# Kernel optimization log

Hardware: AMD Instinct MI355X
Metric: run time of the kernel (lower is better)

## Reference

```python
import jax, jax.numpy as jnp
import numpy as np

MOMENTUM = 0.999
TEMP = 0.07
NUM_HARD_NEGS = 16
NUM_CLASSES = 20000


def _normalize(x, axis=-1, eps=1e-12):
    n = jnp.linalg.norm(x, axis=axis, keepdims=True)
    return x / jnp.maximum(n, eps)


def setup_inputs() -> dict:
    key = jax.random.key(0)
    k1, k2, k3, k4, k5 = jax.random.split(key, 5)
    B, K, Dp, De, C = 512, 8, 256, 512, NUM_CLASSES
    return {
        "part_features": jax.random.normal(k1, (B, K, Dp), dtype=jnp.float32),
        "embeddings": jax.random.normal(k2, (B, De), dtype=jnp.float32),
        "sat_emb": jax.random.normal(k3, (B, De), dtype=jnp.float32),
        "part_bank": jax.random.normal(k4, (C, K, Dp), dtype=jnp.float32) * 0.01,
        "embed_bank": jax.random.normal(k5, (C, De), dtype=jnp.float32) * 0.01,
        "labels": jnp.arange(B, dtype=jnp.int64),
    }


def reference(part_features, embeddings, sat_emb, part_bank, embed_bank, labels):
    m = MOMENTUM
    B = embeddings.shape[0]
    C = embed_bank.shape[0]

    # --- EMA scatter update (bank assumed initialized for all classes) ---
    # labels are distinct, so vectorized scatter == sequential python loop.
    new_part_bank = part_bank.at[labels].set(
        m * part_bank[labels] + (1.0 - m) * part_features)
    new_embed_bank = embed_bank.at[labels].set(
        m * embed_bank[labels] + (1.0 - m) * embeddings)

    # Banks are torch buffers updated under no_grad -> stop_gradient.
    eb = jax.lax.stop_gradient(new_embed_bank)

    # --- PrototypeNCE ---
    q = _normalize(embeddings)                      # [B, De]
    protos = _normalize(eb)                         # [C, De]
    sim = (q @ protos.T) / TEMP                     # [B, C]
    pos_sim = jnp.take_along_axis(sim, labels[:, None], axis=1)  # [B, 1]
    class_ids = jnp.arange(C)
    pos_mask = labels[:, None] == class_ids[None, :]
    neg_sim = jnp.where(pos_mask, -1e9, sim)
    hard_negs, _ = jax.lax.top_k(neg_sim, NUM_HARD_NEGS)          # [B, k]
    logits = jnp.concatenate([pos_sim, hard_negs], axis=1)       # [B, 1+k]
    nce_loss = jnp.mean(jax.nn.logsumexp(logits, axis=1) - logits[:, 0])

    # --- Cross-view prototype alignment ---
    p = _normalize(eb[labels])                      # [B, De]
    d = _normalize(embeddings)
    s = _normalize(sat_emb)
    align_loss = 0.5 * (jnp.mean(1.0 - jnp.sum(d * p, axis=-1))
                        + jnp.mean(1.0 - jnp.sum(s * p, axis=-1)))

    return new_part_bank, new_embed_bank, nce_loss, align_loss
```

## Files before the change

kernel.cpp:

```cpp
#include <hip/hip_runtime.h>
#include <math.h>

#define MOM 0.999f
#define ONE_M_MOM 0.001f
#define INV_TEMP (1.0f / 0.07f)
#define C_CLASSES 20000
#define B_SZ 512
#define DE 512
#define PART_ROW 2048
#define PART_BANK_N (C_CLASSES * PART_ROW)
#define EMB_BANK_N (C_CLASSES * DE)
#define NEG_INF (-3.0e38f)
#define NTILE 157
#define NGEMM (4 * NTILE)
#define NCHUNK 2500

typedef __attribute__((ext_vector_type(8))) short short8;
typedef __attribute__((ext_vector_type(4))) float f32x4;

__device__ inline unsigned short f2bf_rne(float f) {
    unsigned u = __builtin_bit_cast(unsigned, f);
    return (unsigned short)((u + 0x7FFFu + ((u >> 16) & 1u)) >> 16);
}

__device__ inline float bf2f(unsigned short u) {
    return __builtin_bit_cast(float, (unsigned)u << 16);
}

__device__ inline void gload16(const void* g, void* l) {
    __builtin_amdgcn_global_load_lds(
        (const __attribute__((address_space(1))) unsigned int*)g,
        (__attribute__((address_space(3))) unsigned int*)l, 16, 0, 0);
}

__global__ void __launch_bounds__(256)
embed_qnorm(const float* __restrict__ ebank, const float* __restrict__ emb,
            const int* __restrict__ labels, float* __restrict__ out_eb,
            float* __restrict__ inv_norm, unsigned short* __restrict__ Ab,
            int* __restrict__ counter) {
    int blk = blockIdx.x;
    int t = threadIdx.x;
    if (blk == 0 && t == 0) *counter = 0;
    int w = t >> 6, l = t & 63;
    if (blk < 5000) {
        int c = blk * 4 + w;
        int m = -1;
#pragma unroll
        for (int k = 0; k < 8; ++k)
            if (labels[l + k * 64] == c) m = l + k * 64;
#pragma unroll
        for (int off = 32; off; off >>= 1) m = max(m, __shfl_xor(m, off));

        const float4* row = (const float4*)(ebank + ((long)c << 9));
        float4 v0 = row[2 * l], v1 = row[2 * l + 1];
        if (m >= 0) {
            const float4* nr = (const float4*)(emb + ((long)m << 9));
            float4 n0 = nr[2 * l], n1 = nr[2 * l + 1];
            v0.x = MOM * v0.x + ONE_M_MOM * n0.x;
            v0.y = MOM * v0.y + ONE_M_MOM * n0.y;
            v0.z = MOM * v0.z + ONE_M_MOM * n0.z;
            v0.w = MOM * v0.w + ONE_M_MOM * n0.w;
            v1.x = MOM * v1.x + ONE_M_MOM * n1.x;
            v1.y = MOM * v1.y + ONE_M_MOM * n1.y;
            v1.z = MOM * v1.z + ONE_M_MOM * n1.z;
            v1.w = MOM * v1.w + ONE_M_MOM * n1.w;
        }
        float4* orow = (float4*)(out_eb + ((long)c << 9));
        orow[2 * l] = v0; orow[2 * l + 1] = v1;
        float ss = v0.x * v0.x + v0.y * v0.y + v0.z * v0.z + v0.w * v0.w
                 + v1.x * v1.x + v1.y * v1.y + v1.z * v1.z + v1.w * v1.w;
#pragma unroll
        for (int off = 32; off; off >>= 1) ss += __shfl_xor(ss, off);
        if (l == 0) inv_norm[c] = 1.0f / fmaxf(sqrtf(ss), 1e-12f);
    } else {
        int b = (blk - 5000) * 4 + w;
        const float4* row = (const float4*)(emb + ((long)b << 9));
        float4 v0 = row[2 * l], v1 = row[2 * l + 1];
        float ss = v0.x * v0.x + v0.y * v0.y + v0.z * v0.z + v0.w * v0.w
                 + v1.x * v1.x + v1.y * v1.y + v1.z * v1.z + v1.w * v1.w;
#pragma unroll
        for (int off = 32; off; off >>= 1) ss += __shfl_xor(ss, off);
        float inv = 1.0f / fmaxf(sqrtf(ss), 1e-12f);
        v0.x *= inv; v0.y *= inv; v0.z *= inv; v0.w *= inv;
        v1.x *= inv; v1.y *= inv; v1.z *= inv; v1.w *= inv;
        short8 o;
        o[0] = (short)f2bf_rne(v0.x); o[1] = (short)f2bf_rne(v0.y);
        o[2] = (short)f2bf_rne(v0.z); o[3] = (short)f2bf_rne(v0.w);
        o[4] = (short)f2bf_rne(v1.x); o[5] = (short)f2bf_rne(v1.y);
        o[6] = (short)f2bf_rne(v1.z); o[7] = (short)f2bf_rne(v1.w);
        *(short8*)(Ab + ((long)b << 9) + l * 8) = o;
    }
}

__global__ void __launch_bounds__(256)
part_gemm(const unsigned short* __restrict__ A, const float* __restrict__ out_eb,
          const float* __restrict__ inv_norm, const int* __restrict__ labels,
          float* __restrict__ partials,
          const float* __restrict__ pb, const float* __restrict__ pf,
          float* __restrict__ out_pb) {
    __shared__ unsigned short smem[128 * 130];

    if (blockIdx.x >= NGEMM) {
        int c0 = (blockIdx.x - NGEMM) * 8;
        int t = threadIdx.x;
        int* mbs = (int*)smem;
        if (t < 8) mbs[t] = -1;
        __syncthreads();
        int la = labels[t], lb = labels[t + 256];
#pragma unroll
        for (int r = 0; r < 8; ++r) {
            if (la == c0 + r) mbs[r] = t;
            if (lb == c0 + r) mbs[r] = t + 256;
        }
        __syncthreads();
        const f32x4* src = (const f32x4*)pb + (long)c0 * (PART_ROW / 4);
        f32x4* dst = (f32x4*)out_pb + (long)c0 * (PART_ROW / 4);
        const f32x4* pf4 = (const f32x4*)pf;
        f32x4 v[16];
#pragma unroll
        for (int i = 0; i < 16; ++i)
            v[i] = __builtin_nontemporal_load(&src[t + i * 256]);
#pragma unroll
        for (int i = 0; i < 16; ++i) {
            int mb = mbs[i >> 1];
            if (mb >= 0) {
                f32x4 n = pf4[(long)mb * (PART_ROW / 4) + (t + (i & 1) * 256)];
                v[i] = MOM * v[i] + ONE_M_MOM * n;
            }
            __builtin_nontemporal_store(v[i], &dst[t + i * 256]);
        }
        return;
    }

    unsigned short* Asm = smem;
    unsigned short* Bsm = smem + 8192;

    const int t = threadIdx.x;
    const int w = t >> 6, l = t & 63;
    const int wr = w >> 1, wc = w & 1;

    int id = blockIdx.x;
    int xcd = id & 7, idx = id >> 3;
    int wg = (xcd < 4) ? xcd * 79 + idx : 316 + (xcd - 4) * 78 + idx;
    const int bm = wg & 3, bn = wg >> 2;

    f32x4 acc[4][4] = {};

    const int srow = t >> 3;
    const long swz = ((t & 7) ^ (srow & 7)) << 3;
    const unsigned short* Ag = A + ((long)(bm * 128 + srow) << 9) + swz;
    char* Adst = (char*)Asm + (w << 10);

    const int brow = t >> 1;
    const int bh = t & 1;
    int gbr = bn * 128 + brow; if (gbr > C_CLASSES - 1) gbr = C_CLASSES - 1;
    const float4* Bsrc = (const float4*)out_eb + ((long)gbr << 7);
    unsigned short* Bwp = Bsm + (brow << 6);

    const int fr = l & 15;
    const int s4 = l >> 4;
    const int swr0 = ((s4) ^ (fr & 7)) << 4;
    const int swr1 = ((4 + s4) ^ (fr & 7)) << 4;

    for (int kt = 0; kt < 8; ++kt) {
        const int ko = kt << 6;
#pragma unroll
        for (int i = 0; i < 4; ++i)
            gload16(Ag + ko + ((long)i << 14), Adst + (i << 12));
        float4 bv[8];
#pragma unroll
        for (int i = 0; i < 8; ++i) bv[i] = Bsrc[kt * 16 + bh * 8 + i];
#pragma unroll
        for (int s = 0; s < 4; ++s) {
            short8 o;
            float4 x0 = bv[2 * s], x1 = bv[2 * s + 1];
            o[0] = (short)f2bf_rne(x0.x); o[1] = (short)f2bf_rne(x0.y);
            o[2] = (short)f2bf_rne(x0.z); o[3] = (short)f2bf_rne(x0.w);
            o[4] = (short)f2bf_rne(x1.x); o[5] = (short)f2bf_rne(x1.y);
            o[6] = (short)f2bf_rne(x1.z); o[7] = (short)f2bf_rne(x1.w);
            int slot = (bh * 4 + s) ^ (brow & 7);
            *(short8*)(Bwp + slot * 8) = o;
        }
        __syncthreads();
        short8 af[2][4], bf[2][4];
        const char* Abase = (const char*)Asm;
        const char* Bbase = (const char*)Bsm;
#pragma unroll
        for (int m = 0; m < 4; ++m) {
            int ra = (wr * 64 + m * 16 + fr) << 7;
            int rb = (wc * 64 + m * 16 + fr) << 7;
            af[0][m] = *(const short8*)(Abase + ra + swr0);
            af[1][m] = *(const short8*)(Abase + ra + swr1);
            bf[0][m] = *(const short8*)(Bbase + rb + swr0);
            bf[1][m] = *(const short8*)(Bbase + rb + swr1);
        }
        __builtin_amdgcn_s_setprio(1);
#pragma unroll
        for (int kk = 0; kk < 2; ++kk)
#pragma unroll
            for (int m = 0; m < 4; ++m)
#pragma unroll
                for (int n = 0; n < 4; ++n)
                    acc[m][n] = __builtin_amdgcn_mfma_f32_16x16x32_bf16(
                        af[kk][m], bf[kk][n], acc[m][n], 0, 0, 0);
        __builtin_amdgcn_s_setprio(0);
        __syncthreads();
    }

    unsigned short* stile = smem;
    const int r4 = s4 << 2;
#pragma unroll
    for (int n = 0; n < 4; ++n) {
        int ct = wc * 64 + fr + n * 16;
        int cg = bn * 128 + ct;
        bool ok = cg < C_CLASSES;
        float sc = ok ? inv_norm[cg] * INV_TEMP : 0.0f;
#pragma unroll
        for (int m = 0; m < 4; ++m) {
            int rt = wr * 64 + r4 + m * 16;
#pragma unroll
            for (int j = 0; j < 4; ++j) {
                float v = ok ? acc[m][n][j] * sc : NEG_INF;
                stile[(rt + j) * 130 + ct] = f2bf_rne(v);
            }
        }
    }
    __syncthreads();

    const int r = t >> 1, half = t & 1;
    const int gr = bm * 128 + r;
    const int lab = labels[gr];
    const int lab_l = lab - (bn << 7) - (half << 6);
    const unsigned short* bp = stile + r * 130 + half * 64;
    float tl[16];
#pragma unroll
    for (int j = 0; j < 16; ++j) tl[j] = NEG_INF;
    for (int c = 0; c < 64; ++c) {
        if (c == lab_l) continue;
        float v = bf2f(bp[c]);
        if (v > tl[15]) {
            tl[15] = v;
#pragma unroll
            for (int j = 15; j > 0; --j) {
                float a = tl[j - 1], bb = tl[j];
                if (bb > a) { tl[j - 1] = bb; tl[j] = a; }
            }
        }
    }
    float ol[16];
#pragma unroll
    for (int j = 0; j < 16; ++j) ol[j] = __shfl_xor(tl[j], 1);
    if (half == 0) {
        float4 o0, o1, o2, o3;
        o0.x = fmaxf(tl[0],  ol[15]); o0.y = fmaxf(tl[1],  ol[14]);
        o0.z = fmaxf(tl[2],  ol[13]); o0.w = fmaxf(tl[3],  ol[12]);
        o1.x = fmaxf(tl[4],  ol[11]); o1.y = fmaxf(tl[5],  ol[10]);
        o1.z = fmaxf(tl[6],  ol[9]);  o1.w = fmaxf(tl[7],  ol[8]);
        o2.x = fmaxf(tl[8],  ol[7]);  o2.y = fmaxf(tl[9],  ol[6]);
        o2.z = fmaxf(tl[10], ol[5]);  o2.w = fmaxf(tl[11], ol[4]);
        o3.x = fmaxf(tl[12], ol[3]);  o3.y = fmaxf(tl[13], ol[2]);
        o3.z = fmaxf(tl[14], ol[1]);  o3.w = fmaxf(tl[15], ol[0]);
        float4* op4 = (float4*)(partials + ((long)gr * NTILE + bn) * 16);
        op4[0] = o0; op4[1] = o1; op4[2] = o2; op4[3] = o3;
    }
}

__global__ void __launch_bounds__(64)
merge_fin(const float* __restrict__ partials, const float* __restrict__ emb,
          const float* __restrict__ out_eb, const float* __restrict__ sat,
          const float* __restrict__ inv_norm, const int* __restrict__ labels,
          float* __restrict__ lnce, float* __restrict__ lalign,
          int* __restrict__ counter, float* __restrict__ out_losses) {
    int b = blockIdx.x;
    int l = threadIdx.x;
    const float4* pr4 = (const float4*)(partials + (long)b * (NTILE * 16));

    float tl[16];
#pragma unroll
    for (int j = 0; j < 16; ++j) tl[j] = NEG_INF;
    for (int i = l; i < NTILE * 4; i += 64) {
        float4 v4 = pr4[i];
        float vv[4] = {v4.x, v4.y, v4.z, v4.w};
#pragma unroll
        for (int q = 0; q < 4; ++q) {
            float v = vv[q];
            if (v > tl[15]) {
                tl[15] = v;
#pragma unroll
                for (int j = 15; j > 0; --j) {
                    float a = tl[j - 1], bb = tl[j];
                    if (bb > a) { tl[j - 1] = bb; tl[j] = a; }
                }
            }
        }
    }

    float M = 0.f, S = 0.f;
#pragma unroll 1
    for (int j = 0; j < 16; ++j) {
        float v = tl[0];
        float mx = v;
#pragma unroll
        for (int off = 32; off; off >>= 1) mx = fmaxf(mx, __shfl_xor(mx, off));
        unsigned long long ball = __ballot(v == mx);
        int win = (int)(__ffsll((unsigned long long)ball)) - 1;
        if (l == win) {
#pragma unroll
            for (int q = 0; q < 15; ++q) tl[q] = tl[q + 1];
            tl[15] = NEG_INF;
        }
        if (j == 0) { M = mx; S = 1.0f; }
        else S += expf(mx - M);
    }

    int lab = labels[b];
    const float4* qr = (const float4*)(emb + ((long)b << 9));
    const float4* er = (const float4*)(out_eb + ((long)lab << 9));
    const float4* sr = (const float4*)(sat + ((long)b << 9));
    float a1 = 0.f, a2 = 0.f, a3 = 0.f, a4 = 0.f;
#pragma unroll
    for (int rr = 0; rr < 2; ++rr) {
        int j = 2 * l + rr;
        float4 d4 = qr[j], s4 = sr[j], e4 = er[j];
        a1 += d4.x * e4.x + d4.y * e4.y + d4.z * e4.z + d4.w * e4.w;
        a2 += s4.x * e4.x + s4.y * e4.y + s4.z * e4.z + s4.w * e4.w;
        a3 += s4.x * s4.x + s4.y * s4.y + s4.z * s4.z + s4.w * s4.w;
        a4 += d4.x * d4.x + d4.y * d4.y + d4.z * d4.z + d4.w * d4.w;
    }
#pragma unroll
    for (int off = 32; off; off >>= 1) {
        a1 += __shfl_xor(a1, off);
        a2 += __shfl_xor(a2, off);
        a3 += __shfl_xor(a3, off);
        a4 += __shfl_xor(a4, off);
    }
    int done = 0;
    if (l == 0) {
        float invl = inv_norm[lab];
        float invq = 1.0f / fmaxf(sqrtf(a4), 1e-12f);
        float pos = a1 * invq * invl * INV_TEMP;
        float mx2 = fmaxf(M, pos);
        float ssum = expf(M - mx2) * S + expf(pos - mx2);
        lnce[b] = logf(ssum) + mx2 - pos;
        float pd = a1 * invq * invl;
        float ps = a2 * invl / fmaxf(sqrtf(a3), 1e-12f);
        lalign[b] = 1.0f - 0.5f * (pd + ps);
        __threadfence();
        done = (atomicAdd(counter, 1) == B_SZ - 1) ? 1 : 0;
    }
    done = __shfl(done, 0);
    if (done) {
        __threadfence();
        volatile const float* vn = lnce;
        volatile const float* va = lalign;
        float s1 = 0.f, s2 = 0.f;
#pragma unroll
        for (int k = 0; k < B_SZ / 64; ++k) {
            s1 += vn[l + k * 64];
            s2 += va[l + k * 64];
        }
#pragma unroll
        for (int off = 32; off; off >>= 1) {
            s1 += __shfl_xor(s1, off);
            s2 += __shfl_xor(s2, off);
        }
        if (l == 0) {
            out_losses[0] = s1 / (float)B_SZ;
            out_losses[1] = s2 / (float)B_SZ;
            *counter = 0;
        }
    }
}

extern "C" void kernel_launch(void* const* d_in, const int* in_sizes, int n_in,
                              void* d_out, int out_size, void* d_ws, size_t ws_size,
                              hipStream_t stream) {
    const float* pf = (const float*)d_in[0];
    const float* emb = (const float*)d_in[1];
    const float* sat = (const float*)d_in[2];
    const float* pb = (const float*)d_in[3];
    const float* ebank = (const float*)d_in[4];
    const int* labels = (const int*)d_in[5];

    float* out = (float*)d_out;
    float* out_pb = out;
    float* out_eb = out + PART_BANK_N;
    float* out_losses = out + PART_BANK_N + EMB_BANK_N;

    float* ws = (float*)d_ws;
    float* inv_norm = ws;
    int* counter = (int*)(inv_norm + C_CLASSES);
    float* lnce = (float*)(counter + 16);
    float* lalign = lnce + B_SZ;
    float* partials = lalign + B_SZ;
    unsigned short* Ab = (unsigned short*)(partials + (long)B_SZ * NTILE * 16);

    embed_qnorm<<<5000 + 128, 256, 0, stream>>>(ebank, emb, labels, out_eb,
                                                inv_norm, Ab, counter);
    part_gemm<<<NGEMM + NCHUNK, 256, 0, stream>>>(Ab, out_eb, inv_norm, labels,
                                                  partials, pb, pf, out_pb);
    merge_fin<<<B_SZ, 64, 0, stream>>>(partials, emb, out_eb, sat, inv_norm,
                                       labels, lnce, lalign, counter, out_losses);
}
```

Measured before the change: 131.2 us.

## Fuse embed-bank EMA, normalization and GEMM into one kernel launch

Merges the embed-bank update/normalization kernel into the GEMM kernel. GEMM blocks now read raw fp32 embeddings and bank rows, apply the EMA update on the fly, convert to bf16 and compute row norms locally, instead of reading a pre-normalized bf16 A buffer and the updated bank written by a prior launch. This removes a kernel boundary and the dependency on inv_norm, letting the bank-copy, EMA and GEMM work overlap. In exchange the A operand is re-read in fp32 and re-converted by every GEMM block rather than loaded once as bf16 via direct-to-LDS loads, and the embed-bank blocks still run as extra blocks in the same grid.

New measurement: 159.3 us. 1.21x slower.

```diff
diff --git a/kernel.cpp b/kernel.cpp
--- a/kernel.cpp
+++ b/kernel.cpp
@@ -14,6 +14,7 @@
 #define NTILE 157
 #define NGEMM (4 * NTILE)
 #define NCHUNK 2500
+#define NEMB 5000
 
 typedef __attribute__((ext_vector_type(8))) short short8;
 typedef __attribute__((ext_vector_type(4))) float f32x4;
@@ -27,23 +28,55 @@
     return __builtin_bit_cast(float, (unsigned)u << 16);
 }
 
-__device__ inline void gload16(const void* g, void* l) {
-    __builtin_amdgcn_global_load_lds(
-        (const __attribute__((address_space(1))) unsigned int*)g,
-        (__attribute__((address_space(3))) unsigned int*)l, 16, 0, 0);
-}
-
 __global__ void __launch_bounds__(256)
-embed_qnorm(const float* __restrict__ ebank, const float* __restrict__ emb,
-            const int* __restrict__ labels, float* __restrict__ out_eb,
-            float* __restrict__ inv_norm, unsigned short* __restrict__ Ab,
-            int* __restrict__ counter) {
-    int blk = blockIdx.x;
-    int t = threadIdx.x;
+fused_all(const float* __restrict__ emb, const float* __restrict__ ebank,
+          const int* __restrict__ labels,
+          const float* __restrict__ pb, const float* __restrict__ pf,
+          float* __restrict__ out_pb, float* __restrict__ out_eb,
+          float* __restrict__ inv_norm, float* __restrict__ partials,
+          int* __restrict__ counter) {
+    __shared__ unsigned short smem[128 * 130];
+    __shared__ int labs[B_SZ];
+    __shared__ int mrow[128];
+    __shared__ float invAl[128], invBl[128];
+
+    const int blk = blockIdx.x;
+    const int t = threadIdx.x;
     if (blk == 0 && t == 0) *counter = 0;
-    int w = t >> 6, l = t & 63;
-    if (blk < 5000) {
-        int c = blk * 4 + w;
+
+    if (blk >= NGEMM && blk < NGEMM + NCHUNK) {
+        int c0 = (blk - NGEMM) * 8;
+        if (t < 8) mrow[t] = -1;
+        __syncthreads();
+        int la = labels[t], lb = labels[t + 256];
+#pragma unroll
+        for (int r = 0; r < 8; ++r) {
+            if (la == c0 + r) mrow[r] = t;
+            if (lb == c0 + r) mrow[r] = t + 256;
+        }
+        __syncthreads();
+        const f32x4* src = (const f32x4*)pb + (long)c0 * (PART_ROW / 4);
+        f32x4* dst = (f32x4*)out_pb + (long)c0 * (PART_ROW / 4);
+        const f32x4* pf4 = (const f32x4*)pf;
+        f32x4 v[16];
+#pragma unroll
+        for (int i = 0; i < 16; ++i)
+            v[i] = __builtin_nontemporal_load(&src[t + i * 256]);
+#pragma unroll
+        for (int i = 0; i < 16; ++i) {
+            int mb = mrow[i >> 1];
+            if (mb >= 0) {
+                f32x4 n = pf4[(long)mb * (PART_ROW / 4) + (t + (i & 1) * 256)];
+                v[i] = MOM * v[i] + ONE_M_MOM * n;
+            }
+            __builtin_nontemporal_store(v[i], &dst[t + i * 256]);
+        }
+        return;
+    }
+
+    if (blk >= NGEMM + NCHUNK) {
+        int w = t >> 6, l = t & 63;
+        int c = (blk - NGEMM - NCHUNK) * 4 + w;
         int m = -1;
 #pragma unroll
         for (int k = 0; k < 8; ++k)
@@ -72,114 +105,87 @@
 #pragma unroll
         for (int off = 32; off; off >>= 1) ss += __shfl_xor(ss, off);
         if (l == 0) inv_norm[c] = 1.0f / fmaxf(sqrtf(ss), 1e-12f);
-    } else {
-        int b = (blk - 5000) * 4 + w;
-        const float4* row = (const float4*)(emb + ((long)b << 9));
-        float4 v0 = row[2 * l], v1 = row[2 * l + 1];
-        float ss = v0.x * v0.x + v0.y * v0.y + v0.z * v0.z + v0.w * v0.w
-                 + v1.x * v1.x + v1.y * v1.y + v1.z * v1.z + v1.w * v1.w;
-#pragma unroll
-        for (int off = 32; off; off >>= 1) ss += __shfl_xor(ss, off);
-        float inv = 1.0f / fmaxf(sqrtf(ss), 1e-12f);
-        v0.x *= inv; v0.y *= inv; v0.z *= inv; v0.w *= inv;
-        v1.x *= inv; v1.y *= inv; v1.z *= inv; v1.w *= inv;
-        short8 o;
-        o[0] = (short)f2bf_rne(v0.x); o[1] = (short)f2bf_rne(v0.y);
-        o[2] = (short)f2bf_rne(v0.z); o[3] = (short)f2bf_rne(v0.w);
-        o[4] = (short)f2bf_rne(v1.x); o[5] = (short)f2bf_rne(v1.y);
-        o[6] = (short)f2bf_rne(v1.z); o[7] = (short)f2bf_rne(v1.w);
-        *(short8*)(Ab + ((long)b << 9) + l * 8) = o;
-    }
-}
-
-__global__ void __launch_bounds__(256)
-part_gemm(const unsigned short* __restrict__ A, const float* __restrict__ out_eb,
-          const float* __restrict__ inv_norm, const int* __restrict__ labels,
-          float* __restrict__ partials,
-          const float* __restrict__ pb, const float* __restrict__ pf,
-          float* __restrict__ out_pb) {
-    __shared__ unsigned short smem[128 * 130];
-
-    if (blockIdx.x >= NGEMM) {
-        int c0 = (blockIdx.x - NGEMM) * 8;
-        int t = threadIdx.x;
-        int* mbs = (int*)smem;
-        if (t < 8) mbs[t] = -1;
-        __syncthreads();
-        int la = labels[t], lb = labels[t + 256];
-#pragma unroll
-        for (int r = 0; r < 8; ++r) {
-            if (la == c0 + r) mbs[r] = t;
-            if (lb == c0 + r) mbs[r] = t + 256;
-        }
-        __syncthreads();
-        const f32x4* src = (const f32x4*)pb + (long)c0 * (PART_ROW / 4);
-        f32x4* dst = (f32x4*)out_pb + (long)c0 * (PART_ROW / 4);
-        const f32x4* pf4 = (const f32x4*)pf;
-        f32x4 v[16];
-#pragma unroll
-        for (int i = 0; i < 16; ++i)
-            v[i] = __builtin_nontemporal_load(&src[t + i * 256]);
-#pragma unroll
-        for (int i = 0; i < 16; ++i) {
-            int mb = mbs[i >> 1];
-            if (mb >= 0) {
-                f32x4 n = pf4[(long)mb * (PART_ROW / 4) + (t + (i & 1) * 256)];
-                v[i] = MOM * v[i] + ONE_M_MOM * n;
-            }
-            __builtin_nontemporal_store(v[i], &dst[t + i * 256]);
-        }
         return;
     }
 
     unsigned short* Asm = smem;
     unsigned short* Bsm = smem + 8192;
 
-    const int t = threadIdx.x;
     const int w = t >> 6, l = t & 63;
     const int wr = w >> 1, wc = w & 1;
 
-    int id = blockIdx.x;
+    int id = blk;
     int xcd = id & 7, idx = id >> 3;
     int wg = (xcd < 4) ? xcd * 79 + idx : 316 + (xcd - 4) * 78 + idx;
     const int bm = wg & 3, bn = wg >> 2;
 
+    labs[t] = labels[t];
+    labs[t + 256] = labels[t + 256];
+    if (t < 128) mrow[t] = -1;
+    __syncthreads();
+    {
+        int la = labs[t], lb2 = labs[t + 256];
+        int r0 = la - bn * 128;
+        if (r0 >= 0 && r0 < 128) mrow[r0] = t;
+        int r1 = lb2 - bn * 128;
+        if (r1 >= 0 && r1 < 128) mrow[r1] = t + 256;
+    }
+    __syncthreads();
+
     f32x4 acc[4][4] = {};
 
-    const int srow = t >> 3;
-    const long swz = ((t & 7) ^ (srow & 7)) << 3;
-    const unsigned short* Ag = A + ((long)(bm * 128 + srow) << 9) + swz;
-    char* Adst = (char*)Asm + (w << 10);
-
-    const int brow = t >> 1;
-    const int bh = t & 1;
-    int gbr = bn * 128 + brow; if (gbr > C_CLASSES - 1) gbr = C_CLASSES - 1;
-    const float4* Bsrc = (const float4*)out_eb + ((long)gbr << 7);
-    unsigned short* Bwp = Bsm + (brow << 6);
+    const int srow = t >> 1, sh = t & 1;
+    const float4* Asrc = (const float4*)emb + ((long)(bm * 128 + srow) << 7);
+    int gbr = bn * 128 + srow; if (gbr > C_CLASSES - 1) gbr = C_CLASSES - 1;
+    const float4* Bsrc = (const float4*)ebank + ((long)gbr << 7);
+    const int mb = mrow[srow];
+    const float4* Esrc = (mb >= 0) ? (const float4*)emb + ((long)mb << 7) : Bsrc;
+    unsigned short* Awp = Asm + (srow << 6);
+    unsigned short* Bwp = Bsm + (srow << 6);
 
     const int fr = l & 15;
     const int s4 = l >> 4;
     const int swr0 = ((s4) ^ (fr & 7)) << 4;
     const int swr1 = ((4 + s4) ^ (fr & 7)) << 4;
 
+    float ssA = 0.f, ssB = 0.f;
+
     for (int kt = 0; kt < 8; ++kt) {
-        const int ko = kt << 6;
-#pragma unroll
-        for (int i = 0; i < 4; ++i)
-            gload16(Ag + ko + ((long)i << 14), Adst + (i << 12));
-        float4 bv[8];
-#pragma unroll
-        for (int i = 0; i < 8; ++i) bv[i] = Bsrc[kt * 16 + bh * 8 + i];
+        const int kof = kt * 16 + sh * 8;
+        float4 av[8], bv[8];
+#pragma unroll
+        for (int i = 0; i < 8; ++i) { av[i] = Asrc[kof + i]; bv[i] = Bsrc[kof + i]; }
+        if (mb >= 0) {
+#pragma unroll
+            for (int i = 0; i < 8; ++i) {
+                float4 n = Esrc[kof + i];
+                bv[i].x = MOM * bv[i].x + ONE_M_MOM * n.x;
+                bv[i].y = MOM * bv[i].y + ONE_M_MOM * n.y;
+                bv[i].z = MOM * bv[i].z + ONE_M_MOM * n.z;
+                bv[i].w = MOM * bv[i].w + ONE_M_MOM * n.w;
+            }
+        }
+#pragma unroll
+        for (int i = 0; i < 8; ++i) {
+            ssA += av[i].x * av[i].x + av[i].y * av[i].y + av[i].z * av[i].z + av[i].w * av[i].w;
+            ssB += bv[i].x * bv[i].x + bv[i].y * bv[i].y + bv[i].z * bv[i].z + bv[i].w * bv[i].w;
+        }
 #pragma unroll
         for (int s = 0; s < 4; ++s) {
-            short8 o;
-            float4 x0 = bv[2 * s], x1 = bv[2 * s + 1];
-            o[0] = (short)f2bf_rne(x0.x); o[1] = (short)f2bf_rne(x0.y);
-            o[2] = (short)f2bf_rne(x0.z); o[3] = (short)f2bf_rne(x0.w);
-            o[4] = (short)f2bf_rne(x1.x); o[5] = (short)f2bf_rne(x1.y);
-            o[6] = (short)f2bf_rne(x1.z); o[7] = (short)f2bf_rne(x1.w);
-            int slot = (bh * 4 + s) ^ (brow & 7);
-            *(short8*)(Bwp + slot * 8) = o;
+            int slot = (sh * 4 + s) ^ (srow & 7);
+            short8 oa, ob;
+            float4 a0 = av[2 * s], a1 = av[2 * s + 1];
+            float4 b0 = bv[2 * s], b1 = bv[2 * s + 1];
+            oa[0] = (short)f2bf_rne(a0.x); oa[1] = (short)f2bf_rne(a0.y);
+            oa[2] = (short)f2bf_rne(a0.z); oa[3] = (short)f2bf_rne(a0.w);
+            oa[4] = (short)f2bf_rne(a1.x); oa[5] = (short)f2bf_rne(a1.y);
+            oa[6] = (short)f2bf_rne(a1.z); oa[7] = (short)f2bf_rne(a1.w);
+            ob[0] = (short)f2bf_rne(b0.x); ob[1] = (short)f2bf_rne(b0.y);
+            ob[2] = (short)f2bf_rne(b0.z); ob[3] = (short)f2bf_rne(b0.w);
+            ob[4] = (short)f2bf_rne(b1.x); ob[5] = (short)f2bf_rne(b1.y);
+            ob[6] = (short)f2bf_rne(b1.z); ob[7] = (short)f2bf_rne(b1.w);
+            *(short8*)(Awp + slot * 8) = oa;
+            *(short8*)(Bwp + slot * 8) = ob;
         }
         __syncthreads();
         short8 af[2][4], bf[2][4];
@@ -207,6 +213,16 @@
         __syncthreads();
     }
 
+    {
+        float oA = __shfl_xor(ssA, 1);
+        float oB = __shfl_xor(ssB, 1);
+        if (sh == 0) {
+            invAl[srow] = 1.0f / fmaxf(sqrtf(ssA + oA), 1e-12f);
+            invBl[srow] = 1.0f / fmaxf(sqrtf(ssB + oB), 1e-12f);
+        }
+    }
+    __syncthreads();
+
     unsigned short* stile = smem;
     const int r4 = s4 << 2;
 #pragma unroll
@@ -214,13 +230,13 @@
         int ct = wc * 64 + fr + n * 16;
         int cg = bn * 128 + ct;
         bool ok = cg < C_CLASSES;
-        float sc = ok ? inv_norm[cg] * INV_TEMP : 0.0f;
+        float sc = ok ? invBl[ct] * INV_TEMP : 0.0f;
 #pragma unroll
         for (int m = 0; m < 4; ++m) {
             int rt = wr * 64 + r4 + m * 16;
 #pragma unroll
             for (int j = 0; j < 4; ++j) {
-                float v = ok ? acc[m][n][j] * sc : NEG_INF;
+                float v = ok ? acc[m][n][j] * sc * invAl[rt + j] : NEG_INF;
                 stile[(rt + j) * 130 + ct] = f2bf_rne(v);
             }
         }
@@ -229,7 +245,7 @@
 
     const int r = t >> 1, half = t & 1;
     const int gr = bm * 128 + r;
-    const int lab = labels[gr];
+    const int lab = labs[gr & 511];
     const int lab_l = lab - (bn << 7) - (half << 6);
     const unsigned short* bp = stile + r * 130 + half * 64;
     float tl[16];
@@ -393,12 +409,9 @@
     float* lnce = (float*)(counter + 16);
     float* lalign = lnce + B_SZ;
     float* partials = lalign + B_SZ;
-    unsigned short* Ab = (unsigned short*)(partials + (long)B_SZ * NTILE * 16);
-
-    embed_qnorm<<<5000 + 128, 256, 0, stream>>>(ebank, emb, labels, out_eb,
-                                                inv_norm, Ab, counter);
-    part_gemm<<<NGEMM + NCHUNK, 256, 0, stream>>>(Ab, out_eb, inv_norm, labels,
-                                                  partials, pb, pf, out_pb);
+
+    fused_all<<<NGEMM + NCHUNK + NEMB, 256, 0, stream>>>(
+        emb, ebank, labels, pb, pf, out_pb, out_eb, inv_norm, partials, counter);
     merge_fin<<<B_SZ, 64, 0, stream>>>(partials, emb, out_eb, sat, inv_norm,
                                        labels, lnce, lalign, counter, out_losses);
 }
```
